# Kernel tuning notes

Hardware: AMD Instinct MI355X
Metric: run time of the kernel (lower is better)

Reference implementation:

```python
import jax, jax.numpy as jnp
import numpy as np

B, K, V = 8192, 1024, 2


def setup_inputs() -> dict:
    key = jax.random.key(0)
    k1, k2, k3, k4, k5, k6 = jax.random.split(key, 6)
    z = jax.random.normal(k1, (B, K), dtype=jnp.float32)
    # -1 means no intervention for that sample
    intervention_target = jax.random.randint(k2, (B,), -1, K)
    intervention_variant = jax.random.randint(k3, (B,), 0, V)
    raw_adjacency = jax.random.normal(k4, (K, K), dtype=jnp.float32) * 0.05
    intervention_means = jax.random.normal(k5, (K, V), dtype=jnp.float32)
    intervention_log_scales = jax.random.normal(k6, (K, V), dtype=jnp.float32) * 0.1
    return {
        "z": z,
        "intervention_target": intervention_target,
        "intervention_variant": intervention_variant,
        "raw_adjacency": raw_adjacency,
        "intervention_means": intervention_means,
        "intervention_log_scales": intervention_log_scales,
    }


def _scm_forward(z, target, variant, raw_adjacency, means, log_scales):
    Kd = z.shape[1]
    # strictly-lower-triangular adjacency (row j holds parents of node j)
    A = raw_adjacency * jnp.tril(jnp.ones((Kd, Kd), z.dtype), k=-1)

    def step(u, xs):
        a_row, mean_row, logsc_row, z_j, j = xs
        # forward substitution: u_j = z_j + sum_{i<j} A[j,i] * u_i
        # columns >= j of u are still zero and A row is zero there too
        value = z_j + u @ a_row  # [B]
        # intervention overwrite for samples with target == j
        m = mean_row[variant]                 # [B]
        s = jnp.exp(logsc_row[variant])       # [B]
        value = jnp.where(target == j, m + s * z_j, value)
        u = jax.lax.dynamic_update_slice(u, value[:, None], (0, j))
        return u, None

    u0 = jnp.zeros_like(z)
    xs = (A, means, log_scales, z.T, jnp.arange(Kd))
    u, _ = jax.lax.scan(step, u0, xs)
    return u


def reference(z, intervention_target, intervention_variant, raw_adjacency,
              intervention_means, intervention_log_scales):
    return _scm_forward(z, intervention_target, intervention_variant,
                        raw_adjacency, intervention_means, intervention_log_scales)
```

## Files before the change

### kernel.cpp

```cpp
#include <hip/hip_runtime.h>
#include <hip/hip_bf16.h>
#include <cstdint>

#define KDIM 1024
#define BDIM 8192
#define VDIM 2
#define NBLK 16

typedef __attribute__((ext_vector_type(8))) short short8;
typedef __attribute__((ext_vector_type(4))) float f32x4;

__device__ inline unsigned short f2bf(float x) {
  unsigned u = __builtin_bit_cast(unsigned, x);
  u = (u + 0x7FFFu + ((u >> 16) & 1u)) >> 16;
  return (unsigned short)u;
}


#define STAGE_T(DST, SRC, ROW0, COL0, LD)                                   \
  {                                                                         \
    const float* _s = (SRC);                                                \
    _Pragma("unroll") for (int _p = 0; _p < 4; ++_p) {                      \
      const int _m = _p * 16 + rw;                                          \
      float4 _v = *(const float4*)(_s + (size_t)((ROW0) + _m) * (LD) +      \
                                   (COL0) + 4 * k4);                        \
      (DST)[4 * k4 + 0][_m] = _v.x;                                         \
      (DST)[4 * k4 + 1][_m] = _v.y;                                         \
      (DST)[4 * k4 + 2][_m] = _v.z;                                         \
      (DST)[4 * k4 + 3][_m] = _v.w;                                         \
    }                                                                       \
  }

#define STAGE_D(DST, SRC, ROW0, COL0, LD)                                   \
  {                                                                         \
    const float* _s = (SRC);                                                \
    _Pragma("unroll") for (int _p = 0; _p < 4; ++_p) {                      \
      const int _kk = _p * 16 + rw;                                         \
      *(float4*)&(DST)[_kk][4 * k4] =                                       \
          *(const float4*)(_s + (size_t)((ROW0) + _kk) * (LD) + (COL0) +    \
                           4 * k4);                                         \
    }                                                                       \
  }

#define ZERO_ACC                                                            \
  _Pragma("unroll") for (int _a = 0; _a < 4; ++_a)                          \
      _Pragma("unroll") for (int _b = 0; _b < 4; ++_b) acc[_a][_b] = 0.f;

__device__ __forceinline__ void mac64(const float (*Ls)[68],
                                      const float (*Rs)[68], int tm, int tn,
                                      float acc[4][4]) {
#pragma unroll 4
  for (int k = 0; k < 64; ++k) {
    const float4 av = *(const float4*)&Ls[k][4 * tm];
    const float4 bv = *(const float4*)&Rs[k][4 * tn];
    const float aa[4] = {av.x, av.y, av.z, av.w};
    const float bb4[4] = {bv.x, bv.y, bv.z, bv.w};
#pragma unroll
    for (int a = 0; a < 4; ++a)
#pragma unroll
      for (int b = 0; b < 4; ++b) acc[a][b] += aa[a] * bb4[b];
  }
}

#define STORE_MT(R0, C0)                                                    \
  _Pragma("unroll") for (int _a = 0; _a < 4; ++_a) {                        \
    *(float4*)(MT + (size_t)((R0) + 4 * tm + _a) * KDIM + (C0) + 4 * tn) =  \
        make_float4(acc[_a][0], acc[_a][1], acc[_a][2], acc[_a][3]);        \
  }

#define MBF_TILE(R0, C0, BUF)                                               \
  {                                                                         \
    __syncthreads();                                                        \
    _Pragma("unroll") for (int _a = 0; _a < 4; ++_a)                        \
        _Pragma("unroll") for (int _b = 0; _b < 4; ++_b)                    \
            (BUF)[4 * tm + _a][4 * tn + _b] = acc[_a][_b];                  \
    __syncthreads();                                                        \
    const int _tr = tid >> 4, _tc = tid & 15;                               \
    _Pragma("unroll") for (int _p = 0; _p < 4; ++_p) {                      \
      const int _il = _p * 16 + _tr;                                        \
      ushort4 _o;                                                           \
      _o.x = f2bf((BUF)[4 * _tc + 0][_il]);                                 \
      _o.y = f2bf((BUF)[4 * _tc + 1][_il]);                                 \
      _o.z = f2bf((BUF)[4 * _tc + 2][_il]);                                 \
      _o.w = f2bf((BUF)[4 * _tc + 3][_il]);                                 \
      *(ushort4*)(Mbf + (size_t)((C0) + _il) * KDIM + (R0) + 4 * _tc) = _o; \
    }                                                                       \
  }

__global__ __launch_bounds__(256) void prep(const float* __restrict__ A,
                                            float* __restrict__ MT,
                                            unsigned short* __restrict__ Mbf,
                                            const float* __restrict__ Z,
                                            unsigned short* __restrict__ Zbf,
                                            int do_zbf) {
  __shared__ float As[64 * 64];
  const int bid = blockIdx.x;

  if (bid < NBLK) {
    const int base = bid * 64;
    for (int i = threadIdx.x; i < 64 * 64; i += 256)
      As[i] = A[(size_t)(base + (i >> 6)) * KDIM + base + (i & 63)];
    __syncthreads();
    if (threadIdx.x < 64) {
      const int c = threadIdx.x;
      float m[64];
#pragma unroll
      for (int r = 0; r < 64; ++r) m[r] = (r == c) ? 1.f : 0.f;
#pragma unroll
      for (int r = 1; r < 64; ++r) {
        float acc0 = 0.f, acc1 = 0.f;
#pragma unroll
        for (int i = 0; i < 64; ++i) {
          if (i >= r) break;
          if (i & 1) acc1 += As[r * 64 + i] * m[i];
          else       acc0 += As[r * 64 + i] * m[i];
        }
        const float v = acc0 + acc1;
        m[r] = (r > c) ? v : m[r];
      }
#pragma unroll
      for (int r = 0; r < 64; r += 4) {
        float4 v = make_float4(m[r], m[r + 1], m[r + 2], m[r + 3]);
        *(float4*)(MT + (size_t)(base + c) * KDIM + base + r) = v;
      }
#pragma unroll
      for (int r = 0; r < 64; ++r)
        Mbf[(size_t)(base + r) * KDIM + base + c] = f2bf(m[r]);
    }
    return;
  }

  const int wid = bid - NBLK;
  const int nw = gridDim.x - NBLK;
  const int idx0 = wid * 256 + threadIdx.x;
  const int stride = nw * 256;
  const float4 z4 = make_float4(0.f, 0.f, 0.f, 0.f);

  for (int i = idx0; i < 240 * 1024; i += stride) {
    const int blk = i >> 10, off = i & 1023;
    const int bi = blk / 15;
    int bj = blk % 15;
    bj += (bj >= bi);
    *(float4*)(MT + (size_t)(bi * 64 + (off >> 4)) * KDIM + bj * 64 +
               4 * (off & 15)) = z4;
  }
  const uint4 u4 = make_uint4(0u, 0u, 0u, 0u);
  for (int i = idx0; i < 240 * 512; i += stride) {
    const int blk = i >> 9, off = i & 511;
    const int bi = blk / 15;
    int bj = blk % 15;
    bj += (bj >= bi);
    *(uint4*)(Mbf + (size_t)(bi * 64 + (off >> 3)) * KDIM + bj * 64 +
              8 * (off & 7)) = u4;
  }
  if (do_zbf) {
    for (int i = idx0; i < BDIM * KDIM / 4; i += stride) {
      float4 v = *(const float4*)(Z + 4 * (size_t)i);
      ushort4 o;
      o.x = f2bf(v.x);
      o.y = f2bf(v.y);
      o.z = f2bf(v.z);
      o.w = f2bf(v.w);
      *(ushort4*)(Zbf + 4 * (size_t)i) = o;
    }
  }
}

__global__ __launch_bounds__(256) void comb01(const float* __restrict__ A,
                                              float* __restrict__ MT,
                                              unsigned short* __restrict__ Mbf) {
  int b = blockIdx.x;
  const int rt = b & 1;
  const int jt = (b >> 1) & 1;
  const int s = b >> 2;
  const int base = s * 256;

  __shared__ float Ls[64][68];
  __shared__ float Rs[64][68];
  __shared__ float tQ0L[64][68];
  __shared__ float tQ0H[64][68];
  __shared__ float tP0[64][68];
  __shared__ float tP1[64][68];

  const int tid = threadIdx.x;
  const int k4 = tid & 15;
  const int rw = tid >> 4;
  const int tm = tid >> 4;
  const int tn = tid & 15;
  float acc[4][4];

  if (jt == 0) {
    STAGE_T(Ls, MT, base, base, KDIM);
    STAGE_T(Rs, A, base + 64, base, KDIM);
    __syncthreads();
    ZERO_ACC;
    mac64(Ls, Rs, tm, tn, acc);
    __syncthreads();
#pragma unroll
    for (int a = 0; a < 4; ++a)
#pragma unroll
      for (int b2 = 0; b2 < 4; ++b2) tP0[4 * tn + b2][4 * tm + a] = acc[a][b2];
    STAGE_D(Rs, MT, base + 64, base + 64, KDIM);
    __syncthreads();
    ZERO_ACC;
    mac64(tP0, Rs, tm, tn, acc);
    __syncthreads();
#pragma unroll
    for (int a = 0; a < 4; ++a)
#pragma unroll
      for (int b2 = 0; b2 < 4; ++b2) tQ0L[4 * tn + b2][4 * tm + a] = acc[a][b2];
    if (rt == 0) {
      STORE_MT(base, base + 64);
      MBF_TILE(base, base + 64, Rs);
    }
  }
  __syncthreads();

  if (rt == 1) {
    STAGE_T(Ls, MT, base + 128, base + 128, KDIM);
    STAGE_T(Rs, A, base + 192, base + 128, KDIM);
    __syncthreads();
    ZERO_ACC;
    mac64(Ls, Rs, tm, tn, acc);
    __syncthreads();
#pragma unroll
    for (int a = 0; a < 4; ++a)
#pragma unroll
      for (int b2 = 0; b2 < 4; ++b2) tP1[4 * tn + b2][4 * tm + a] = acc[a][b2];
    STAGE_D(Rs, MT, base + 192, base + 192, KDIM);
    __syncthreads();
    ZERO_ACC;
    mac64(tP1, Rs, tm, tn, acc);
    __syncthreads();
#pragma unroll
    for (int a = 0; a < 4; ++a)
#pragma unroll
      for (int b2 = 0; b2 < 4; ++b2) tQ0H[4 * tm + a][4 * tn + b2] = acc[a][b2];
    if (jt == 1) {
      STORE_MT(base + 128, base + 192);
      MBF_TILE(base + 128, base + 192, Rs);
    }
  }
  __syncthreads();

  STAGE_T(Ls, MT, base + 64 * jt, base + 64 * jt, KDIM);
  __syncthreads();
  for (int kb2 = 0; kb2 <= rt; ++kb2) {
    ZERO_ACC;
    for (int kb = jt; kb < 2; ++kb) {
      STAGE_T(Rs, A, base + 128 + 64 * kb2, base + 64 * kb, KDIM);
      __syncthreads();
      mac64(kb == jt ? Ls : tQ0L, Rs, tm, tn, acc);
      __syncthreads();
    }
    if (kb2 == 0) {
#pragma unroll
      for (int a = 0; a < 4; ++a)
#pragma unroll
        for (int b2 = 0; b2 < 4; ++b2) tP0[4 * tn + b2][4 * tm + a] = acc[a][b2];
    } else {
#pragma unroll
      for (int a = 0; a < 4; ++a)
#pragma unroll
        for (int b2 = 0; b2 < 4; ++b2) tP1[4 * tn + b2][4 * tm + a] = acc[a][b2];
    }
  }
  __syncthreads();

  ZERO_ACC;
  if (rt == 0) {
    STAGE_D(Rs, MT, base + 128, base + 128, KDIM);
    __syncthreads();
    mac64(tP0, Rs, tm, tn, acc);
    __syncthreads();
  } else {
    mac64(tP0, tQ0H, tm, tn, acc);
    __syncthreads();
    STAGE_D(Rs, MT, base + 192, base + 192, KDIM);
    __syncthreads();
    mac64(tP1, Rs, tm, tn, acc);
    __syncthreads();
  }
  STORE_MT(base + 64 * jt, base + 128 + 64 * rt);
  MBF_TILE(base + 64 * jt, base + 128 + 64 * rt, Rs);
}

template <int T>
__global__ __launch_bounds__(256) void p_k(const float* __restrict__ A,
                                           const float* __restrict__ MT,
                                           float* __restrict__ Pt) {
  int b = blockIdx.x;
  const int rb = b % T; b /= T;
  const int jb = b % T; b /= T;
  const int c = b;
  const int h = 64 * T;
  const int base = c * 2 * h;

  __shared__ float Ls[64][68];
  __shared__ float Rs[64][68];
  const int tid = threadIdx.x;
  const int k4 = tid & 15;
  const int rw = tid >> 4;
  const int tm = tid >> 4;
  const int tn = tid & 15;
  float acc[4][4];
  ZERO_ACC;

  for (int kb = jb; kb < T; ++kb) {
    STAGE_T(Ls, MT, base + 64 * jb, base + 64 * kb, KDIM);
    STAGE_T(Rs, A, base + h + 64 * rb, base + 64 * kb, KDIM);
    __syncthreads();
    mac64(Ls, Rs, tm, tn, acc);
    __syncthreads();
  }

  float* P0 = Pt + (size_t)c * h * h;
#pragma unroll
  for (int a = 0; a < 4; ++a)
    *(float4*)(P0 + (size_t)(64 * jb + 4 * tm + a) * h + 64 * rb + 4 * tn) =
        make_float4(acc[a][0], acc[a][1], acc[a][2], acc[a][3]);
}

template <int T>
__global__ __launch_bounds__(256) void q_k(float* __restrict__ MT,
                                           const float* __restrict__ Pt,
                                           unsigned short* __restrict__ Mbf) {
  int b = blockIdx.x;
  const int rb = b % T; b /= T;
  const int jb = b % T; b /= T;
  const int c = b;
  const int h = 64 * T;
  const int base = c * 2 * h;

  __shared__ float Ls[64][68];
  __shared__ float Rs[64][68];
  const int tid = threadIdx.x;
  const int k4 = tid & 15;
  const int rw = tid >> 4;
  const int tm = tid >> 4;
  const int tn = tid & 15;
  float acc[4][4];
  ZERO_ACC;

  const float* P0 = Pt + (size_t)c * h * h;
  for (int kb = 0; kb <= rb; ++kb) {
    STAGE_T(Ls, P0, 64 * jb, 64 * kb, h);
    STAGE_D(Rs, MT, base + h + 64 * kb, base + h + 64 * rb, KDIM);
    __syncthreads();
    mac64(Ls, Rs, tm, tn, acc);
    __syncthreads();
  }

  STORE_MT(base + 64 * jb, base + h + 64 * rb);
  MBF_TILE(base + 64 * jb, base + h + 64 * rb, Ls);
}

#define LDB 72

template <int ZBF>
__global__ __launch_bounds__(256) void gemm_mfma(
    const float* __restrict__ Z, const unsigned short* __restrict__ Zbf,
    const unsigned short* __restrict__ Mbf, float* __restrict__ C) {
  __shared__ unsigned short As[128][LDB];
  __shared__ unsigned short Bs[128][LDB];

  const int d = blockIdx.x;
  const int xbl = d & 7;
  const int nir = (d >> 3) & 7;
  const int xbh = d >> 6;
  const int xb = xbh * 8 + xbl;
  const int ni = (xb & 32) ? (7 - nir) : nir;
  const int b0 = xb * 128;
  const int i0 = ni * 128;

  const int tid = threadIdx.x;
  const int w = tid >> 6;
  const int lane = tid & 63;
  const int wr = w >> 1, wc = w & 1;
  const int mlane = lane & 15;
  const int q = lane >> 4;

  const int rq = tid >> 4, kq = tid & 15;
  const int cb = tid >> 3, ck = tid & 7;

  f32x4 acc[4][4];
#pragma unroll
  for (int a = 0; a < 4; ++a)
#pragma unroll
    for (int b = 0; b < 4; ++b) acc[a][b] = (f32x4){0.f, 0.f, 0.f, 0.f};

  const int nkb = 2 * (ni + 1);
  for (int kb = 0; kb < nkb; ++kb) {
    const int k0 = kb * 64;
    if (ZBF) {
#pragma unroll
      for (int p = 0; p < 4; ++p) {
        const int r = p * 32 + cb;
        *(uint4*)&As[r][8 * ck] =
            *(const uint4*)(Zbf + (size_t)(b0 + r) * KDIM + k0 + 8 * ck);
      }
    } else {
#pragma unroll
      for (int p = 0; p < 8; ++p) {
        const int r = p * 16 + rq;
        float4 zv = *(const float4*)(Z + (size_t)(b0 + r) * KDIM + k0 + 4 * kq);
        ushort4 o;
        o.x = f2bf(zv.x);
        o.y = f2bf(zv.y);
        o.z = f2bf(zv.z);
        o.w = f2bf(zv.w);
        *(ushort4*)&As[r][4 * kq] = o;
      }
    }
#pragma unroll
    for (int p = 0; p < 4; ++p) {
      const int c = p * 32 + cb;
      *(uint4*)&Bs[c][8 * ck] =
          *(const uint4*)(Mbf + (size_t)(i0 + c) * KDIM + k0 + 8 * ck);
    }
    __syncthreads();
#pragma unroll
    for (int ks = 0; ks < 2; ++ks) {
      const int kf = ks * 32 + q * 8;
      short8 av[4], bv[4];
#pragma unroll
      for (int a = 0; a < 4; ++a)
        av[a] = *(const short8*)&As[wr * 64 + 16 * a + mlane][kf];
#pragma unroll
      for (int b = 0; b < 4; ++b)
        bv[b] = *(const short8*)&Bs[wc * 64 + 16 * b + mlane][kf];
#pragma unroll
      for (int a = 0; a < 4; ++a)
#pragma unroll
        for (int b = 0; b < 4; ++b)
          acc[a][b] =
              __builtin_amdgcn_mfma_f32_16x16x32_bf16(av[a], bv[b], acc[a][b], 0, 0, 0);
    }
    __syncthreads();
  }

#pragma unroll
  for (int a = 0; a < 4; ++a) {
    const int row0 = b0 + wr * 64 + 16 * a + q * 4;
#pragma unroll
    for (int b = 0; b < 4; ++b) {
      const int col = i0 + wc * 64 + 16 * b + mlane;
      float* Cp = C + (size_t)row0 * KDIM + col;
      Cp[0 * KDIM] = acc[a][b][0];
      Cp[1 * KDIM] = acc[a][b][1];
      Cp[2 * KDIM] = acc[a][b][2];
      Cp[3 * KDIM] = acc[a][b][3];
    }
  }
}

__global__ __launch_bounds__(256) void correction_k(
    const float* __restrict__ z, const int* __restrict__ tgt,
    const int* __restrict__ var, const float* __restrict__ means,
    const float* __restrict__ lsc, const float* __restrict__ MT,
    float* __restrict__ out) {
  const int b = blockIdx.x;
  const int t = tgt[b];
  if (t < 0) return;
  const int v = var[b];
  const float mval = means[t * VDIM + v];
  const float sval = expf(lsc[t * VDIM + v]);
  const float zv = z[(size_t)b * KDIM + t];
  const float gt = out[(size_t)b * KDIM + t];
  const float coef = (mval + sval * zv) - gt;
  __syncthreads();
  const int i = threadIdx.x * 4;
  float4 g = *(float4*)(out + (size_t)b * KDIM + i);
  float4 mt = *(const float4*)(MT + (size_t)t * KDIM + i);
  g.x += coef * mt.x;
  g.y += coef * mt.y;
  g.z += coef * mt.z;
  g.w += coef * mt.w;
  *(float4*)(out + (size_t)b * KDIM + i) = g;
}

extern "C" void kernel_launch(void* const* d_in, const int* in_sizes, int n_in,
                              void* d_out, int out_size, void* d_ws,
                              size_t ws_size, hipStream_t stream) {
  const float* z = (const float*)d_in[0];
  const int* tgt = (const int*)d_in[1];
  const int* var = (const int*)d_in[2];
  const float* A = (const float*)d_in[3];
  const float* means = (const float*)d_in[4];
  const float* lsc = (const float*)d_in[5];
  float* out = (float*)d_out;

  char* ws = (char*)d_ws;
  float* MT = (float*)ws;
  unsigned short* Mbf = (unsigned short*)(ws + (4u << 20));
  float* Pt2 = (float*)(ws + (6u << 20));
  float* Pt3 = (float*)(ws + (6u << 20) + (512u << 10));
  unsigned short* Zbf = (unsigned short*)(ws + (7u << 20) + (512u << 10));
  const int use_zbf =
      ws_size >= (7u << 20) + (512u << 10) + (size_t)BDIM * KDIM * 2 ? 1 : 0;

  hipLaunchKernelGGL(prep, dim3(512), dim3(256), 0, stream, A, MT, Mbf, z, Zbf,
                     use_zbf);
  hipLaunchKernelGGL(comb01, dim3(16), dim3(256), 0, stream, A, MT, Mbf);
  hipLaunchKernelGGL((p_k<4>), dim3(32), dim3(256), 0, stream, A, MT, Pt2);
  hipLaunchKernelGGL((q_k<4>), dim3(32), dim3(256), 0, stream, MT, Pt2, Mbf);
  hipLaunchKernelGGL((p_k<8>), dim3(64), dim3(256), 0, stream, A, MT, Pt3);
  hipLaunchKernelGGL((q_k<8>), dim3(64), dim3(256), 0, stream, MT, Pt3, Mbf);
  if (use_zbf)
    hipLaunchKernelGGL((gemm_mfma<1>), dim3((BDIM / 128) * (KDIM / 128)),
                       dim3(256), 0, stream, z, Zbf, Mbf, out);
  else
    hipLaunchKernelGGL((gemm_mfma<0>), dim3((BDIM / 128) * (KDIM / 128)),
                       dim3(256), 0, stream, z, Zbf, Mbf, out);
  hipLaunchKernelGGL(correction_k, dim3(BDIM), dim3(256), 0, stream, z, tgt,
                     var, means, lsc, MT, out);
}
```

Measured before the change: 262.9 us.

## Fuse intervention correction into GEMM epilogue and overlap zero-fill with P-stage

The separate correction kernel is removed. Each GEMM block now recomputes the pre-intervention value at the target column as a dot product of the bf16 z row with the Mbf row, forms the coefficient, and adds coef*MT[target] in the epilogue before storing. That drops a full read-modify-write pass over the output. The zero-fill and z-to-bf16 conversion are also moved out of prep and into the p_k<4> launch, where extra blocks run alongside the 32 compute blocks. In exchange, every GEMM block now does redundant dot products and scattered MT loads, and the correction uses bf16 values instead of the exact fp32 GEMM result at the target column.

```diff
diff --git a/kernel.cpp b/kernel.cpp
--- a/kernel.cpp
+++ b/kernel.cpp
@@ -14,6 +14,10 @@
   unsigned u = __builtin_bit_cast(unsigned, x);
   u = (u + 0x7FFFu + ((u >> 16) & 1u)) >> 16;
   return (unsigned short)u;
+}
+
+__device__ inline float bf2f(unsigned short x) {
+  return __builtin_bit_cast(float, (unsigned)x << 16);
 }
 
 
@@ -87,82 +91,39 @@
     }                                                                       \
   }
 
-__global__ __launch_bounds__(256) void prep(const float* __restrict__ A,
-                                            float* __restrict__ MT,
-                                            unsigned short* __restrict__ Mbf,
-                                            const float* __restrict__ Z,
-                                            unsigned short* __restrict__ Zbf,
-                                            int do_zbf) {
+__global__ __launch_bounds__(256) void prep_inv(const float* __restrict__ A,
+                                                float* __restrict__ MT,
+                                                unsigned short* __restrict__ Mbf) {
   __shared__ float As[64 * 64];
-  const int bid = blockIdx.x;
-
-  if (bid < NBLK) {
-    const int base = bid * 64;
-    for (int i = threadIdx.x; i < 64 * 64; i += 256)
-      As[i] = A[(size_t)(base + (i >> 6)) * KDIM + base + (i & 63)];
-    __syncthreads();
-    if (threadIdx.x < 64) {
-      const int c = threadIdx.x;
-      float m[64];
-#pragma unroll
-      for (int r = 0; r < 64; ++r) m[r] = (r == c) ? 1.f : 0.f;
-#pragma unroll
-      for (int r = 1; r < 64; ++r) {
-        float acc0 = 0.f, acc1 = 0.f;
-#pragma unroll
-        for (int i = 0; i < 64; ++i) {
-          if (i >= r) break;
-          if (i & 1) acc1 += As[r * 64 + i] * m[i];
-          else       acc0 += As[r * 64 + i] * m[i];
-        }
-        const float v = acc0 + acc1;
-        m[r] = (r > c) ? v : m[r];
-      }
-#pragma unroll
-      for (int r = 0; r < 64; r += 4) {
-        float4 v = make_float4(m[r], m[r + 1], m[r + 2], m[r + 3]);
-        *(float4*)(MT + (size_t)(base + c) * KDIM + base + r) = v;
-      }
-#pragma unroll
-      for (int r = 0; r < 64; ++r)
-        Mbf[(size_t)(base + r) * KDIM + base + c] = f2bf(m[r]);
-    }
-    return;
-  }
-
-  const int wid = bid - NBLK;
-  const int nw = gridDim.x - NBLK;
-  const int idx0 = wid * 256 + threadIdx.x;
-  const int stride = nw * 256;
-  const float4 z4 = make_float4(0.f, 0.f, 0.f, 0.f);
-
-  for (int i = idx0; i < 240 * 1024; i += stride) {
-    const int blk = i >> 10, off = i & 1023;
-    const int bi = blk / 15;
-    int bj = blk % 15;
-    bj += (bj >= bi);
-    *(float4*)(MT + (size_t)(bi * 64 + (off >> 4)) * KDIM + bj * 64 +
-               4 * (off & 15)) = z4;
-  }
-  const uint4 u4 = make_uint4(0u, 0u, 0u, 0u);
-  for (int i = idx0; i < 240 * 512; i += stride) {
-    const int blk = i >> 9, off = i & 511;
-    const int bi = blk / 15;
-    int bj = blk % 15;
-    bj += (bj >= bi);
-    *(uint4*)(Mbf + (size_t)(bi * 64 + (off >> 3)) * KDIM + bj * 64 +
-              8 * (off & 7)) = u4;
-  }
-  if (do_zbf) {
-    for (int i = idx0; i < BDIM * KDIM / 4; i += stride) {
-      float4 v = *(const float4*)(Z + 4 * (size_t)i);
-      ushort4 o;
-      o.x = f2bf(v.x);
-      o.y = f2bf(v.y);
-      o.z = f2bf(v.z);
-      o.w = f2bf(v.w);
-      *(ushort4*)(Zbf + 4 * (size_t)i) = o;
-    }
+  const int base = blockIdx.x * 64;
+  for (int i = threadIdx.x; i < 64 * 64; i += 256)
+    As[i] = A[(size_t)(base + (i >> 6)) * KDIM + base + (i & 63)];
+  __syncthreads();
+  if (threadIdx.x < 64) {
+    const int c = threadIdx.x;
+    float m[64];
+#pragma unroll
+    for (int r = 0; r < 64; ++r) m[r] = (r == c) ? 1.f : 0.f;
+#pragma unroll
+    for (int r = 1; r < 64; ++r) {
+      float acc0 = 0.f, acc1 = 0.f;
+#pragma unroll
+      for (int i = 0; i < 64; ++i) {
+        if (i >= r) break;
+        if (i & 1) acc1 += As[r * 64 + i] * m[i];
+        else       acc0 += As[r * 64 + i] * m[i];
+      }
+      const float v = acc0 + acc1;
+      m[r] = (r > c) ? v : m[r];
+    }
+#pragma unroll
+    for (int r = 0; r < 64; r += 4) {
+      float4 v = make_float4(m[r], m[r + 1], m[r + 2], m[r + 3]);
+      *(float4*)(MT + (size_t)(base + c) * KDIM + base + r) = v;
+    }
+#pragma unroll
+    for (int r = 0; r < 64; ++r)
+      Mbf[(size_t)(base + r) * KDIM + base + c] = f2bf(m[r]);
   }
 }
 
@@ -283,6 +244,81 @@
   }
   STORE_MT(base + 64 * jt, base + 128 + 64 * rt);
   MBF_TILE(base + 64 * jt, base + 128 + 64 * rt, Rs);
+}
+
+__global__ __launch_bounds__(256) void p4_stream(
+    const float* __restrict__ A, float* __restrict__ MT,
+    float* __restrict__ Pt, const float* __restrict__ Z,
+    unsigned short* __restrict__ Zbf, unsigned short* __restrict__ Mbf,
+    int do_zbf) {
+  __shared__ float Ls[64][68];
+  __shared__ float Rs[64][68];
+
+  if (blockIdx.x >= 32) {
+    const int wid = blockIdx.x - 32;
+    const int nw = gridDim.x - 32;
+    const int idx0 = wid * 256 + threadIdx.x;
+    const int stride = nw * 256;
+    const float4 z4 = make_float4(0.f, 0.f, 0.f, 0.f);
+    const uint4 u4 = make_uint4(0u, 0u, 0u, 0u);
+
+    for (int i = idx0; i < 256 * 1024; i += stride) {
+      const int blk = i >> 10, off = i & 1023;
+      const int bi = blk >> 4, bj = blk & 15;
+      if (bi <= bj) continue;
+      *(float4*)(MT + (size_t)(bi * 64 + (off >> 4)) * KDIM + bj * 64 +
+                 4 * (off & 15)) = z4;
+    }
+    for (int i = idx0; i < 256 * 512; i += stride) {
+      const int blk = i >> 9, off = i & 511;
+      const int bi = blk >> 4, bj = blk & 15;
+      if (bi >= bj) continue;
+      *(uint4*)(Mbf + (size_t)(bi * 64 + (off >> 3)) * KDIM + bj * 64 +
+                8 * (off & 7)) = u4;
+    }
+    if (do_zbf) {
+      for (int i = idx0; i < BDIM * KDIM / 4; i += stride) {
+        float4 v = *(const float4*)(Z + 4 * (size_t)i);
+        ushort4 o;
+        o.x = f2bf(v.x);
+        o.y = f2bf(v.y);
+        o.z = f2bf(v.z);
+        o.w = f2bf(v.w);
+        *(ushort4*)(Zbf + 4 * (size_t)i) = o;
+      }
+    }
+    return;
+  }
+
+  int b = blockIdx.x;
+  const int T = 4;
+  const int rb = b % T; b /= T;
+  const int jb = b % T; b /= T;
+  const int c = b;
+  const int h = 64 * T;
+  const int base = c * 2 * h;
+
+  const int tid = threadIdx.x;
+  const int k4 = tid & 15;
+  const int rw = tid >> 4;
+  const int tm = tid >> 4;
+  const int tn = tid & 15;
+  float acc[4][4];
+  ZERO_ACC;
+
+  for (int kb = jb; kb < T; ++kb) {
+    STAGE_T(Ls, MT, base + 64 * jb, base + 64 * kb, KDIM);
+    STAGE_T(Rs, A, base + h + 64 * rb, base + 64 * kb, KDIM);
+    __syncthreads();
+    mac64(Ls, Rs, tm, tn, acc);
+    __syncthreads();
+  }
+
+  float* P0 = Pt + (size_t)c * h * h;
+#pragma unroll
+  for (int a = 0; a < 4; ++a)
+    *(float4*)(P0 + (size_t)(64 * jb + 4 * tm + a) * h + 64 * rb + 4 * tn) =
+        make_float4(acc[a][0], acc[a][1], acc[a][2], acc[a][3]);
 }
 
 template <int T>
@@ -360,9 +396,14 @@
 template <int ZBF>
 __global__ __launch_bounds__(256) void gemm_mfma(
     const float* __restrict__ Z, const unsigned short* __restrict__ Zbf,
-    const unsigned short* __restrict__ Mbf, float* __restrict__ C) {
+    const unsigned short* __restrict__ Mbf, const float* __restrict__ MT,
+    const int* __restrict__ tgt, const int* __restrict__ var,
+    const float* __restrict__ means, const float* __restrict__ lsc,
+    float* __restrict__ C) {
   __shared__ unsigned short As[128][LDB];
   __shared__ unsigned short Bs[128][LDB];
+  __shared__ float scoef[128];
+  __shared__ int stb[128];
 
   const int d = blockIdx.x;
   const int xbl = d & 7;
@@ -439,44 +480,82 @@
     __syncthreads();
   }
 
+  {
+    const int s = tid >> 1, h2 = tid & 1;
+    const int br = b0 + s;
+    const int tb = tgt[br];
+    float part = 0.f;
+    if (tb >= 0) {
+      const int nk16 = (tb >> 4) + 1;
+      if (ZBF) {
+        const unsigned short* zr = Zbf + (size_t)br * KDIM;
+        const unsigned short* mr = Mbf + (size_t)tb * KDIM;
+        for (int c16 = h2; c16 < nk16; c16 += 2) {
+          const uint4 za = *(const uint4*)(zr + c16 * 16);
+          const uint4 zb2 = *(const uint4*)(zr + c16 * 16 + 8);
+          const uint4 ma = *(const uint4*)(mr + c16 * 16);
+          const uint4 mb2 = *(const uint4*)(mr + c16 * 16 + 8);
+          const unsigned zw[8] = {za.x, za.y, za.z, za.w,
+                                  zb2.x, zb2.y, zb2.z, zb2.w};
+          const unsigned mw[8] = {ma.x, ma.y, ma.z, ma.w,
+                                  mb2.x, mb2.y, mb2.z, mb2.w};
+#pragma unroll
+          for (int wv = 0; wv < 8; ++wv) {
+            part += __builtin_bit_cast(float, zw[wv] << 16) *
+                    __builtin_bit_cast(float, mw[wv] << 16);
+            part += __builtin_bit_cast(float, zw[wv] & 0xFFFF0000u) *
+                    __builtin_bit_cast(float, mw[wv] & 0xFFFF0000u);
+          }
+        }
+      } else {
+        const float* zr = Z + (size_t)br * KDIM;
+        const unsigned short* mr = Mbf + (size_t)tb * KDIM;
+        const int nk8 = (tb >> 3) + 1;
+        for (int c8 = h2; c8 < nk8; c8 += 2) {
+          const float4 z0 = *(const float4*)(zr + c8 * 8);
+          const float4 z1 = *(const float4*)(zr + c8 * 8 + 4);
+          const ushort4 m0 = *(const ushort4*)(mr + c8 * 8);
+          const ushort4 m1 = *(const ushort4*)(mr + c8 * 8 + 4);
+          part += z0.x * bf2f(m0.x) + z0.y * bf2f(m0.y) + z0.z * bf2f(m0.z) +
+                  z0.w * bf2f(m0.w) + z1.x * bf2f(m1.x) + z1.y * bf2f(m1.y) +
+                  z1.z * bf2f(m1.z) + z1.w * bf2f(m1.w);
+        }
+      }
+    }
+    part += __shfl_down(part, 1);
+    if (h2 == 0) {
+      float cf = 0.f;
+      int tbs = 0;
+      if (tb >= 0) {
+        const int v = var[br];
+        const float mval = means[tb * VDIM + v];
+        const float sval = expf(lsc[tb * VDIM + v]);
+        const float zv = Z[(size_t)br * KDIM + tb];
+        cf = (mval + sval * zv) - part;
+        tbs = tb;
+      }
+      scoef[s] = cf;
+      stb[s] = tbs;
+    }
+  }
+  __syncthreads();
+
 #pragma unroll
   for (int a = 0; a < 4; ++a) {
-    const int row0 = b0 + wr * 64 + 16 * a + q * 4;
+    const int l0 = wr * 64 + 16 * a + q * 4;
+    const int row0 = b0 + l0;
 #pragma unroll
     for (int b = 0; b < 4; ++b) {
       const int col = i0 + wc * 64 + 16 * b + mlane;
       float* Cp = C + (size_t)row0 * KDIM + col;
-      Cp[0 * KDIM] = acc[a][b][0];
-      Cp[1 * KDIM] = acc[a][b][1];
-      Cp[2 * KDIM] = acc[a][b][2];
-      Cp[3 * KDIM] = acc[a][b][3];
-    }
-  }
-}
-
-__global__ __launch_bounds__(256) void correction_k(
-    const float* __restrict__ z, const int* __restrict__ tgt,
-    const int* __restrict__ var, const float* __restrict__ means,
-    const float* __restrict__ lsc, const float* __restrict__ MT,
-    float* __restrict__ out) {
-  const int b = blockIdx.x;
-  const int t = tgt[b];
-  if (t < 0) return;
-  const int v = var[b];
-  const float mval = means[t * VDIM + v];
-  const float sval = expf(lsc[t * VDIM + v]);
-  const float zv = z[(size_t)b * KDIM + t];
-  const float gt = out[(size_t)b * KDIM + t];
-  const float coef = (mval + sval * zv) - gt;
-  __syncthreads();
-  const int i = threadIdx.x * 4;
-  float4 g = *(float4*)(out + (size_t)b * KDIM + i);
-  float4 mt = *(const float4*)(MT + (size_t)t * KDIM + i);
-  g.x += coef * mt.x;
-  g.y += coef * mt.y;
-  g.z += coef * mt.z;
-  g.w += coef * mt.w;
-  *(float4*)(out + (size_t)b * KDIM + i) = g;
+#pragma unroll
+      for (int j = 0; j < 4; ++j) {
+        const float cf = scoef[l0 + j];
+        const float corr = cf * MT[(size_t)stb[l0 + j] * KDIM + col];
+        Cp[j * KDIM] = acc[a][b][j] + corr;
+      }
+    }
+  }
 }
 
 extern "C" void kernel_launch(void* const* d_in, const int* in_sizes, int n_in,
@@ -499,19 +578,19 @@
   const int use_zbf =
       ws_size >= (7u << 20) + (512u << 10) + (size_t)BDIM * KDIM * 2 ? 1 : 0;
 
-  hipLaunchKernelGGL(prep, dim3(512), dim3(256), 0, stream, A, MT, Mbf, z, Zbf,
-                     use_zbf);
+  hipLaunchKernelGGL(prep_inv, dim3(NBLK), dim3(256), 0, stream, A, MT, Mbf);
   hipLaunchKernelGGL(comb01, dim3(16), dim3(256), 0, stream, A, MT, Mbf);
-  hipLaunchKernelGGL((p_k<4>), dim3(32), dim3(256), 0, stream, A, MT, Pt2);
+  hipLaunchKernelGGL(p4_stream, dim3(512), dim3(256), 0, stream, A, MT, Pt2, z,
+                     Zbf, Mbf, use_zbf);
   hipLaunchKernelGGL((q_k<4>), dim3(32), dim3(256), 0, stream, MT, Pt2, Mbf);
   hipLaunchKernelGGL((p_k<8>), dim3(64), dim3(256), 0, stream, A, MT, Pt3);
   hipLaunchKernelGGL((q_k<8>), dim3(64), dim3(256), 0, stream, MT, Pt3, Mbf);
   if (use_zbf)
     hipLaunchKernelGGL((gemm_mfma<1>), dim3((BDIM / 128) * (KDIM / 128)),
-                       dim3(256), 0, stream, z, Zbf, Mbf, out);
+                       dim3(256), 0, stream, z, Zbf, Mbf, MT, tgt, var, means,
+                       lsc, out);
   else
     hipLaunchKernelGGL((gemm_mfma<0>), dim3((BDIM / 128) * (KDIM / 128)),
-                       dim3(256), 0, stream, z, Zbf, Mbf, out);
-  hipLaunchKernelGGL(correction_k, dim3(BDIM), dim3(256), 0, stream, z, tgt,
-                     var, means, lsc, MT, out);
-}
+                       dim3(256), 0, stream, z, Zbf, Mbf, MT, tgt, var, means,
+                       lsc, out);
+}
```

Measured after the change: 256.5 us. 2.4% less time.
